# Performance work log

Hardware: AMD Instinct MI355X
Metric: run time of the kernel (lower is better)

Reference implementation:

```python
import jax, jax.numpy as jnp
import numpy as np

N = 50000   # num_entities
F = 300     # node feature dim
D = 128     # embedding_dim
H = 4       # heads
C = D // H  # per-head out channels (32)
E = 640000  # num edges
R = 200     # num_relations
L = 2       # num_layers
NEG_SLOPE = 0.2  # PyG GATv2Conv default


def setup_inputs() -> dict:
    key = jax.random.key(0)
    ks = jax.random.split(key, 14)
    s = 0.1
    return {
        "entity": jnp.arange(N, dtype=jnp.int32),
        "edge_index": jax.random.randint(ks[0], (2, E), 0, N, dtype=jnp.int32),
        "edge_type": jax.random.randint(ks[1], (E,), 0, R, dtype=jnp.int32),
        # learned parameters
        "node_features": jax.random.normal(ks[2], (N, F), jnp.float32) * s,   # entity_embedding table
        "rel_emb": jax.random.normal(ks[3], (R, D), jnp.float32) * s,          # relation_embedding
        "proj_w": jax.random.normal(ks[4], (F, D), jnp.float32) * s,           # project Linear
        "proj_b": jnp.zeros((D,), jnp.float32),
        # per-layer GATv2Conv params, stacked over L layers
        "w_l": jax.random.normal(ks[5], (L, D, H * C), jnp.float32) * s,       # lin_l weight
        "b_l": jnp.zeros((L, H * C), jnp.float32),
        "w_r": jax.random.normal(ks[6], (L, D, H * C), jnp.float32) * s,       # lin_r weight
        "b_r": jnp.zeros((L, H * C), jnp.float32),
        "w_e": jax.random.normal(ks[7], (L, D, H * C), jnp.float32) * s,       # lin_edge weight (no bias)
        "att": jax.random.normal(ks[8], (L, H, C), jnp.float32) * s,           # attention vector a
        "bias": jnp.zeros((L, H * C), jnp.float32),                             # output bias
    }


def _gatv2_layer(x, src, dst, edge_attr, w_l, b_l, w_r, b_r, w_e, att, bias):
    # x: [N, D], edge_attr: [E, D]
    x_l = (x @ w_l + b_l).reshape(N, H, C)
    x_r = (x @ w_r + b_r).reshape(N, H, C)
    e = (edge_attr @ w_e).reshape(E, H, C)
    # per-edge message (gather src/dst + edge), GATv2: leaky_relu BEFORE attention dot
    m = jax.nn.leaky_relu(x_l[src] + x_r[dst] + e, NEG_SLOPE)   # [E, H, C]
    logits = jnp.einsum('ehc,hc->eh', m, att)                    # [E, H]
    # segment softmax over edges grouped by destination node
    lmax = jax.ops.segment_max(logits, dst, num_segments=N)      # [N, H]
    ex = jnp.exp(logits - lmax[dst])                             # [E, H]
    denom = jax.ops.segment_sum(ex, dst, num_segments=N)         # [N, H]
    alpha = ex / denom[dst]                                      # [E, H]
    # scatter-aggregate messages x_l[src] weighted by alpha
    out = jax.ops.segment_sum(x_l[src] * alpha[:, :, None], dst, num_segments=N)  # [N, H, C]
    return out.reshape(N, H * C) + bias


def reference(entity, edge_index, edge_type, node_features, rel_emb,
              proj_w, proj_b, w_l, b_l, w_r, b_r, w_e, att, bias):
    x = node_features[entity]            # embedding lookup
    x = x @ proj_w + proj_b              # project to D
    edge_attr = rel_emb[edge_type]       # [E, D] (weights=False -> no edge_weight scaling)
    src, dst = edge_index[0], edge_index[1]
    for i in range(L):
        x = _gatv2_layer(x, src, dst, edge_attr,
                         w_l[i], b_l[i], w_r[i], b_r[i], w_e[i], att[i], bias[i])
        if i != L - 1:
            x = jax.nn.elu(x)            # dropout inactive (eval mode)
    return x
```

## Files before the change

kernel.cpp:

```cpp
#include <hip/hip_runtime.h>

#define NN 50000
#define FF 300
#define DD 128
#define HH 4
#define CC 32
#define EE 640000
#define RR 200
#define LL 2
#define SB ((NN + 255) / 256)
#define PK 320
#define WTOT (128 * PK + 4 * 128 * 128)
#define HB ((EE + 255) / 256)
#define WB ((WTOT + 255) / 256)
#define RB (LL * RR / 2)

typedef unsigned short u16;
typedef unsigned int u32;
typedef __attribute__((ext_vector_type(8))) short short8;
typedef __attribute__((ext_vector_type(4))) float floatx4;

__device__ __forceinline__ float bf2f(u16 u) {
    union { u32 i; float f; } v; v.i = ((u32)u) << 16; return v.f;
}
__device__ __forceinline__ u16 f2bf(float f) {
    u32 u = __float_as_uint(f);
    u32 r = (u >> 16) & 1u;
    u += 0x7fffu + r;
    return (u16)(u >> 16);
}
__device__ __forceinline__ void bf2x(u32 p, float& lo, float& hi) {
    lo = __uint_as_float(p << 16);
    hi = __uint_as_float(p & 0xffff0000u);
}

__device__ __forceinline__ int block_excl_scan(int v, int* lds4, int* total) {
    int lane = threadIdx.x & 63, wid = threadIdx.x >> 6;
    int x = v;
    #pragma unroll
    for (int off = 1; off < 64; off <<= 1) {
        int y = __shfl_up(x, off, 64);
        if (lane >= off) x += y;
    }
    if (lane == 63) lds4[wid] = x;
    __syncthreads();
    int add = 0;
    #pragma unroll
    for (int w = 0; w < 4; w++) add += (w < wid) ? lds4[w] : 0;
    *total = lds4[0] + lds4[1] + lds4[2] + lds4[3];
    return x + add - v;
}

__global__ __launch_bounds__(256)
void prep_kernel(const int* __restrict__ ei, int* __restrict__ counts,
                 const float* __restrict__ proj_w, const float* __restrict__ w_l,
                 const float* __restrict__ w_r, u16* __restrict__ wt,
                 const float* __restrict__ rel_emb, const float* __restrict__ w_e,
                 u16* __restrict__ erel)
{
    __shared__ float rv[2][DD];
    int b = blockIdx.x, tid = threadIdx.x;
    if (b < HB) {
        int e = b * 256 + tid;
        if (e < EE) atomicAdd(&counts[ei[EE + e]], 1);
    } else if (b < HB + WB) {
        int i = (b - HB) * 256 + tid;
        if (i < WTOT) {
            float v;
            if (i < 128 * PK) {
                int n = i / PK, k = i - n * PK;
                v = (k < FF) ? proj_w[(size_t)k * DD + n] : 0.f;
            } else {
                int j = i - 128 * PK;
                int seg = j >> 14;
                int r = j & 16383;
                int n = r >> 7, k = r & 127;
                const float* src = (seg < 2) ? (w_l + (size_t)seg * DD * DD)
                                             : (w_r + (size_t)(seg - 2) * DD * DD);
                v = src[(size_t)k * DD + n];
            }
            wt[i] = f2bf(v);
        }
    } else {
        int half = tid >> 7, d = tid & 127;
        int lr = (b - HB - WB) * 2 + half;
        int l = lr / RR, r = lr - l * RR;
        rv[half][d] = rel_emb[r * DD + d];
        __syncthreads();
        const float* W = w_e + (size_t)l * DD * DD;
        float acc = 0.f;
        #pragma unroll 8
        for (int k = 0; k < DD; k++) acc += rv[half][k] * W[k * DD + d];
        erel[(size_t)lr * DD + d] = f2bf(acc);
    }
}

template<bool ABF16, bool GATHER>
__global__ __launch_bounds__(256)
void gemm_mfma_kernel(const void* __restrict__ A_, const int* __restrict__ rowidx,
                      int lda, int K, int Ka, int ldb,
                      const u16* __restrict__ BT1, const float* __restrict__ bias1,
                      u16* __restrict__ C1,
                      const u16* __restrict__ BT2, const float* __restrict__ bias2,
                      u16* __restrict__ C2, int M)
{
    const u16*   BT   = (blockIdx.y == 0) ? BT1 : BT2;
    const float* bias = (blockIdx.y == 0) ? bias1 : bias2;
    u16*         Cout = (blockIdx.y == 0) ? C1 : C2;

    __shared__ u16 As[128][72];
    __shared__ u16 Bs[128][72];
    int tid  = threadIdx.x;
    int m0   = blockIdx.x * 128;
    int wave = tid >> 6, lane = tid & 63;
    int quad = lane >> 4, l16 = lane & 15;
    int wrow = (wave >> 1) * 64, wcol = (wave & 1) * 64;

    floatx4 acc[4][4];
    #pragma unroll
    for (int i = 0; i < 4; i++)
        #pragma unroll
        for (int j = 0; j < 4; j++) acc[i][j] = (floatx4){0.f, 0.f, 0.f, 0.f};

    int ar = tid >> 1, ah = tid & 1;
    int arow = m0 + ar;
    int rid = (arow < M) ? (GATHER ? rowidx[arow] : arow) : 0;

    for (int kk = 0; kk < K; kk += 64) {
        #pragma unroll
        for (int q = 0; q < 2; q++) {
            int kb = kk + ah * 32 + q * 16;
            u16 tmp[16];
            if (ABF16) {
                const u16* Ap = (const u16*)A_ + (size_t)rid * lda + kb;
                if (kb + 16 <= Ka) {
                    *(short8*)&tmp[0] = *(const short8*)Ap;
                    *(short8*)&tmp[8] = *(const short8*)(Ap + 8);
                } else {
                    #pragma unroll
                    for (int j = 0; j < 16; j++) tmp[j] = (kb + j < Ka) ? Ap[j] : (u16)0;
                }
            } else {
                const float* Ap = (const float*)A_ + (size_t)rid * lda + kb;
                if (kb + 16 <= Ka) {
                    #pragma unroll
                    for (int qq = 0; qq < 4; qq++) {
                        float4 f = *(const float4*)(Ap + qq * 4);
                        tmp[qq*4+0] = f2bf(f.x); tmp[qq*4+1] = f2bf(f.y);
                        tmp[qq*4+2] = f2bf(f.z); tmp[qq*4+3] = f2bf(f.w);
                    }
                } else {
                    #pragma unroll
                    for (int j = 0; j < 16; j++) tmp[j] = (kb + j < Ka) ? f2bf(Ap[j]) : (u16)0;
                }
            }
            *(short8*)&As[ar][ah * 32 + q * 16]     = *(short8*)&tmp[0];
            *(short8*)&As[ar][ah * 32 + q * 16 + 8] = *(short8*)&tmp[8];
        }
        {
            const u16* Bp = BT + (size_t)ar * ldb + kk + ah * 32;
            #pragma unroll
            for (int q = 0; q < 4; q++)
                *(short8*)&Bs[ar][ah * 32 + q * 8] = *(const short8*)(Bp + q * 8);
        }
        __syncthreads();
        #pragma unroll
        for (int ks = 0; ks < 2; ks++) {
            short8 af[4], bfr[4];
            #pragma unroll
            for (int i = 0; i < 4; i++)
                af[i] = *(const short8*)&As[wrow + i * 16 + l16][ks * 32 + quad * 8];
            #pragma unroll
            for (int j = 0; j < 4; j++)
                bfr[j] = *(const short8*)&Bs[wcol + j * 16 + l16][ks * 32 + quad * 8];
            #pragma unroll
            for (int i = 0; i < 4; i++)
                #pragma unroll
                for (int j = 0; j < 4; j++)
                    acc[i][j] = __builtin_amdgcn_mfma_f32_16x16x32_bf16(
                        af[i], bfr[j], acc[i][j], 0, 0, 0);
        }
        __syncthreads();
    }

    #pragma unroll
    for (int i = 0; i < 4; i++) {
        #pragma unroll
        for (int rr = 0; rr < 4; rr++) {
            int row = m0 + wrow + i * 16 + quad * 4 + rr;
            if (row < M) {
                #pragma unroll
                for (int j = 0; j < 4; j++) {
                    int col = wcol + j * 16 + l16;
                    Cout[(size_t)row * DD + col] = f2bf(acc[i][j][rr] + bias[col]);
                }
            }
        }
    }
}

__global__ __launch_bounds__(256)
void scan_local_kernel(const int* __restrict__ counts, int* __restrict__ offsets,
                       int* __restrict__ bsum)
{
    __shared__ int lds4[4];
    int i = blockIdx.x * 256 + threadIdx.x;
    int v = (i < NN) ? counts[i] : 0;
    int total;
    int ex = block_excl_scan(v, lds4, &total);
    if (i < NN) offsets[i] = ex;
    if (threadIdx.x == 0) bsum[blockIdx.x] = total;
}

__global__ __launch_bounds__(256)
void scan_bsum_kernel(int* __restrict__ bsum)
{
    __shared__ int lds4[4];
    int t = threadIdx.x;
    int v = (t < SB) ? bsum[t] : 0;
    int total;
    int ex = block_excl_scan(v, lds4, &total);
    if (t < SB) bsum[t] = ex;
}

__global__ __launch_bounds__(256)
void scan_add_kernel(int* __restrict__ offsets, const int* __restrict__ bsum)
{
    int i = blockIdx.x * 256 + threadIdx.x;
    if (i < NN) offsets[i] += bsum[i >> 8];
    if (i == 0) offsets[NN] = EE;
}

__global__ __launch_bounds__(256)
void scatter_kernel(const int* __restrict__ ei, const int* __restrict__ et,
                    const int* __restrict__ offsets,
                    int* __restrict__ fill, u32* __restrict__ dstorder)
{
    int e = blockIdx.x * 256 + threadIdx.x;
    if (e >= EE) return;
    int d = ei[EE + e];
    int pos = offsets[d] + atomicAdd(&fill[d], 1);
    dstorder[pos] = (u32)ei[e] | ((u32)et[e] << 16);
}

__global__ __launch_bounds__(256)
void node_kernel(const u32* __restrict__ dstorder, const int* __restrict__ offsets,
                 const u16* __restrict__ xl, const u16* __restrict__ xr,
                 const u16* __restrict__ erel, const float* __restrict__ att,
                 const float* __restrict__ bias,
                 u16* __restrict__ xnext, float* __restrict__ outp, int is_last)
{
    int tid  = threadIdx.x;
    int node = blockIdx.x * 4 + (tid >> 6);
    int lane = tid & 63;
    if (node >= NN) return;
    int g  = lane >> 4;
    int gl = lane & 15;
    int c0 = gl * 8;
    int beg = offsets[node], end = offsets[node + 1];

    float xrf[8], attf[8];
    {
        const u32* xp = (const u32*)&xr[(size_t)node * DD + c0];
        #pragma unroll
        for (int q = 0; q < 4; q++) bf2x(xp[q], xrf[q*2], xrf[q*2+1]);
        float4 a0 = *(const float4*)&att[c0];
        float4 a1 = *(const float4*)&att[c0 + 4];
        attf[0]=a0.x; attf[1]=a0.y; attf[2]=a0.z; attf[3]=a0.w;
        attf[4]=a1.x; attf[5]=a1.y; attf[6]=a1.z; attf[7]=a1.w;
    }

    float s = 0.f;
    float a[8];
    #pragma unroll
    for (int j = 0; j < 8; j++) a[j] = 0.f;

    for (int base = beg; base < end; base += 4) {
        int es = base + g;
        bool valid = es < end;
        u32 st = valid ? dstorder[es] : 0;
        int src = st & 0xffff;
        int typ = st >> 16;
        const u32* xp = (const u32*)&xl[(size_t)src * DD + c0];
        const u32* ep = (const u32*)&erel[(size_t)typ * DD + c0];
        u32 xv0 = xp[0], xv1 = xp[1], xv2 = xp[2], xv3 = xp[3];
        u32 ev0 = ep[0], ev1 = ep[1], ev2 = ep[2], ev3 = ep[3];
        float xf[8], ef[8];
        bf2x(xv0, xf[0], xf[1]); bf2x(xv1, xf[2], xf[3]);
        bf2x(xv2, xf[4], xf[5]); bf2x(xv3, xf[6], xf[7]);
        bf2x(ev0, ef[0], ef[1]); bf2x(ev1, ef[2], ef[3]);
        bf2x(ev2, ef[4], ef[5]); bf2x(ev3, ef[6], ef[7]);
        float p = 0.f;
        #pragma unroll
        for (int j = 0; j < 8; j++) {
            float m = xf[j] + xrf[j] + ef[j];
            m = fmaxf(m, 0.2f * m);
            p += m * attf[j];
        }
        p += __shfl_xor(p, 1, 64);
        p += __shfl_xor(p, 2, 64);
        float w = valid ? __expf(fminf(p, 60.f)) : 0.f;
        s += w;
        #pragma unroll
        for (int j = 0; j < 8; j++) a[j] += w * xf[j];
    }

    #pragma unroll
    for (int j = 0; j < 8; j++) {
        a[j] += __shfl_xor(a[j], 16, 64);
        a[j] += __shfl_xor(a[j], 32, 64);
    }
    s += __shfl_xor(s, 16, 64);
    s += __shfl_xor(s, 32, 64);

    if (lane < 16) {
        float rh = 1.f / fmaxf(s, 1e-30f);
        float4 b0 = *(const float4*)&bias[c0];
        float4 b1 = *(const float4*)&bias[c0 + 4];
        float bv[8] = {b0.x, b0.y, b0.z, b0.w, b1.x, b1.y, b1.z, b1.w};
        float v[8];
        #pragma unroll
        for (int j = 0; j < 8; j++) v[j] = a[j] * rh + bv[j];
        if (is_last) {
            float4* op = (float4*)&outp[(size_t)node * DD + c0];
            op[0] = make_float4(v[0], v[1], v[2], v[3]);
            op[1] = make_float4(v[4], v[5], v[6], v[7]);
        } else {
            u16 pk[8];
            #pragma unroll
            for (int j = 0; j < 8; j++) {
                float w2 = v[j] > 0.f ? v[j] : __expf(v[j]) - 1.f;
                pk[j] = f2bf(w2);
            }
            *(short8*)&xnext[(size_t)node * DD + c0] = *(short8*)pk;
        }
    }
}

extern "C" void kernel_launch(void* const* d_in, const int* in_sizes, int n_in,
                              void* d_out, int out_size, void* d_ws, size_t ws_size,
                              hipStream_t stream)
{
    const int*   entity        = (const int*)d_in[0];
    const int*   edge_index    = (const int*)d_in[1];
    const int*   edge_type     = (const int*)d_in[2];
    const float* node_features = (const float*)d_in[3];
    const float* rel_emb       = (const float*)d_in[4];
    const float* proj_w        = (const float*)d_in[5];
    const float* proj_b        = (const float*)d_in[6];
    const float* w_l           = (const float*)d_in[7];
    const float* b_l           = (const float*)d_in[8];
    const float* w_r           = (const float*)d_in[9];
    const float* b_r           = (const float*)d_in[10];
    const float* w_e           = (const float*)d_in[11];
    const float* att           = (const float*)d_in[12];
    const float* bias          = (const float*)d_in[13];

    u16*   xb      = (u16*)d_ws;
    u16*   xl      = xb + (size_t)NN * DD;
    u16*   xr      = xl + (size_t)NN * DD;
    u16*   erel    = xr + (size_t)NN * DD;
    u16*   wt      = erel + (size_t)LL * RR * DD;
    u32*   dstorder= (u32*)(wt + WTOT);
    int*   counts  = (int*)(dstorder + (size_t)EE);
    int*   fill    = counts + NN;
    int*   offsets = fill + NN;
    int*   bsum    = offsets + NN + 1;

    hipMemsetAsync(counts, 0, (size_t)NN * 2 * sizeof(int), stream);
    prep_kernel<<<HB + WB + RB, 256, 0, stream>>>(
        edge_index, counts, proj_w, w_l, w_r, wt, rel_emb, w_e, erel);

    scan_local_kernel<<<SB, 256, 0, stream>>>(counts, offsets, bsum);
    scan_bsum_kernel<<<1, 256, 0, stream>>>(bsum);
    scan_add_kernel<<<SB, 256, 0, stream>>>(offsets, bsum);
    scatter_kernel<<<(EE + 255) / 256, 256, 0, stream>>>(
        edge_index, edge_type, offsets, fill, dstorder);

    const u16* wtProj = wt;
    const int GB = (NN + 127) / 128;
    gemm_mfma_kernel<false, true><<<dim3(GB, 1), 256, 0, stream>>>(
        node_features, entity, FF, PK, FF, PK,
        wtProj, proj_b, xb, wtProj, proj_b, xb, NN);

    for (int l = 0; l < LL; l++) {
        const u16* wtl = wt + 128 * PK + l * 16384;
        const u16* wtr = wt + 128 * PK + 32768 + l * 16384;
        gemm_mfma_kernel<true, false><<<dim3(GB, 2), 256, 0, stream>>>(
            xb, nullptr, DD, DD, DD, DD,
            wtl, b_l + l * DD, xl,
            wtr, b_r + l * DD, xr, NN);

        node_kernel<<<(NN + 3) / 4, 256, 0, stream>>>(
            dstorder, offsets, xl, xr, erel + (size_t)l * RR * DD,
            att + (size_t)l * DD, bias + (size_t)l * DD,
            xb, (float*)d_out, l == LL - 1);
    }
}
```

Measured before the change: 338.7 us.

## Store xl and edge embeddings in fp32 and fold block-scan add into consumers

```diff
diff --git a/kernel.cpp b/kernel.cpp
--- a/kernel.cpp
+++ b/kernel.cpp
@@ -56,7 +56,7 @@
                  const float* __restrict__ proj_w, const float* __restrict__ w_l,
                  const float* __restrict__ w_r, u16* __restrict__ wt,
                  const float* __restrict__ rel_emb, const float* __restrict__ w_e,
-                 u16* __restrict__ erel)
+                 float* __restrict__ erel)
 {
     __shared__ float rv[2][DD];
     int b = blockIdx.x, tid = threadIdx.x;
@@ -91,22 +91,21 @@
         float acc = 0.f;
         #pragma unroll 8
         for (int k = 0; k < DD; k++) acc += rv[half][k] * W[k * DD + d];
-        erel[(size_t)lr * DD + d] = f2bf(acc);
-    }
-}
-
-template<bool ABF16, bool GATHER>
+        erel[(size_t)lr * DD + d] = acc;
+    }
+}
+
+template<bool ABF16, bool GATHER, bool OUT1F32>
 __global__ __launch_bounds__(256)
 void gemm_mfma_kernel(const void* __restrict__ A_, const int* __restrict__ rowidx,
                       int lda, int K, int Ka, int ldb,
                       const u16* __restrict__ BT1, const float* __restrict__ bias1,
-                      u16* __restrict__ C1,
+                      void* __restrict__ C1,
                       const u16* __restrict__ BT2, const float* __restrict__ bias2,
                       u16* __restrict__ C2, int M)
 {
     const u16*   BT   = (blockIdx.y == 0) ? BT1 : BT2;
     const float* bias = (blockIdx.y == 0) ? bias1 : bias2;
-    u16*         Cout = (blockIdx.y == 0) ? C1 : C2;
 
     __shared__ u16 As[128][72];
     __shared__ u16 Bs[128][72];
@@ -192,7 +191,13 @@
                 #pragma unroll
                 for (int j = 0; j < 4; j++) {
                     int col = wcol + j * 16 + l16;
-                    Cout[(size_t)row * DD + col] = f2bf(acc[i][j][rr] + bias[col]);
+                    float v = acc[i][j][rr] + bias[col];
+                    if (OUT1F32 && blockIdx.y == 0) {
+                        ((float*)C1)[(size_t)row * DD + col] = v;
+                    } else {
+                        u16* Cb = (blockIdx.y == 0) ? (u16*)C1 : C2;
+                        Cb[(size_t)row * DD + col] = f2bf(v);
+                    }
                 }
             }
         }
@@ -224,29 +229,22 @@
 }
 
 __global__ __launch_bounds__(256)
-void scan_add_kernel(int* __restrict__ offsets, const int* __restrict__ bsum)
-{
-    int i = blockIdx.x * 256 + threadIdx.x;
-    if (i < NN) offsets[i] += bsum[i >> 8];
-    if (i == 0) offsets[NN] = EE;
-}
-
-__global__ __launch_bounds__(256)
 void scatter_kernel(const int* __restrict__ ei, const int* __restrict__ et,
-                    const int* __restrict__ offsets,
+                    const int* __restrict__ offsets, const int* __restrict__ bsum,
                     int* __restrict__ fill, u32* __restrict__ dstorder)
 {
     int e = blockIdx.x * 256 + threadIdx.x;
     if (e >= EE) return;
     int d = ei[EE + e];
-    int pos = offsets[d] + atomicAdd(&fill[d], 1);
+    int pos = offsets[d] + bsum[d >> 8] + atomicAdd(&fill[d], 1);
     dstorder[pos] = (u32)ei[e] | ((u32)et[e] << 16);
 }
 
 __global__ __launch_bounds__(256)
 void node_kernel(const u32* __restrict__ dstorder, const int* __restrict__ offsets,
-                 const u16* __restrict__ xl, const u16* __restrict__ xr,
-                 const u16* __restrict__ erel, const float* __restrict__ att,
+                 const int* __restrict__ bsum,
+                 const float* __restrict__ xl, const u16* __restrict__ xr,
+                 const float* __restrict__ erel, const float* __restrict__ att,
                  const float* __restrict__ bias,
                  u16* __restrict__ xnext, float* __restrict__ outp, int is_last)
 {
@@ -257,7 +255,8 @@
     int g  = lane >> 4;
     int gl = lane & 15;
     int c0 = gl * 8;
-    int beg = offsets[node], end = offsets[node + 1];
+    int beg = offsets[node] + bsum[node >> 8];
+    int end = (node == NN - 1) ? EE : offsets[node + 1] + bsum[(node + 1) >> 8];
 
     float xrf[8], attf[8];
     {
@@ -281,15 +280,14 @@
         u32 st = valid ? dstorder[es] : 0;
         int src = st & 0xffff;
         int typ = st >> 16;
-        const u32* xp = (const u32*)&xl[(size_t)src * DD + c0];
-        const u32* ep = (const u32*)&erel[(size_t)typ * DD + c0];
-        u32 xv0 = xp[0], xv1 = xp[1], xv2 = xp[2], xv3 = xp[3];
-        u32 ev0 = ep[0], ev1 = ep[1], ev2 = ep[2], ev3 = ep[3];
-        float xf[8], ef[8];
-        bf2x(xv0, xf[0], xf[1]); bf2x(xv1, xf[2], xf[3]);
-        bf2x(xv2, xf[4], xf[5]); bf2x(xv3, xf[6], xf[7]);
-        bf2x(ev0, ef[0], ef[1]); bf2x(ev1, ef[2], ef[3]);
-        bf2x(ev2, ef[4], ef[5]); bf2x(ev3, ef[6], ef[7]);
+        const float* xp = xl + (size_t)src * DD + c0;
+        const float* ep = erel + (size_t)typ * DD + c0;
+        float4 x0 = *(const float4*)xp;
+        float4 x1 = *(const float4*)(xp + 4);
+        float4 e0 = *(const float4*)ep;
+        float4 e1 = *(const float4*)(ep + 4);
+        float xf[8] = {x0.x, x0.y, x0.z, x0.w, x1.x, x1.y, x1.z, x1.w};
+        float ef[8] = {e0.x, e0.y, e0.z, e0.w, e1.x, e1.y, e1.z, e1.w};
         float p = 0.f;
         #pragma unroll
         for (int j = 0; j < 8; j++) {
@@ -357,15 +355,15 @@
     const float* bias          = (const float*)d_in[13];
 
     u16*   xb      = (u16*)d_ws;
-    u16*   xl      = xb + (size_t)NN * DD;
-    u16*   xr      = xl + (size_t)NN * DD;
-    u16*   erel    = xr + (size_t)NN * DD;
-    u16*   wt      = erel + (size_t)LL * RR * DD;
+    float* xlf     = (float*)(xb + (size_t)NN * DD);
+    u16*   xr      = (u16*)(xlf + (size_t)NN * DD);
+    float* erel    = (float*)(xr + (size_t)NN * DD);
+    u16*   wt      = (u16*)(erel + (size_t)LL * RR * DD);
     u32*   dstorder= (u32*)(wt + WTOT);
     int*   counts  = (int*)(dstorder + (size_t)EE);
     int*   fill    = counts + NN;
     int*   offsets = fill + NN;
-    int*   bsum    = offsets + NN + 1;
+    int*   bsum    = offsets + NN;
 
     hipMemsetAsync(counts, 0, (size_t)NN * 2 * sizeof(int), stream);
     prep_kernel<<<HB + WB + RB, 256, 0, stream>>>(
@@ -373,26 +371,25 @@
 
     scan_local_kernel<<<SB, 256, 0, stream>>>(counts, offsets, bsum);
     scan_bsum_kernel<<<1, 256, 0, stream>>>(bsum);
-    scan_add_kernel<<<SB, 256, 0, stream>>>(offsets, bsum);
     scatter_kernel<<<(EE + 255) / 256, 256, 0, stream>>>(
-        edge_index, edge_type, offsets, fill, dstorder);
+        edge_index, edge_type, offsets, bsum, fill, dstorder);
 
     const u16* wtProj = wt;
     const int GB = (NN + 127) / 128;
-    gemm_mfma_kernel<false, true><<<dim3(GB, 1), 256, 0, stream>>>(
+    gemm_mfma_kernel<false, true, false><<<dim3(GB, 1), 256, 0, stream>>>(
         node_features, entity, FF, PK, FF, PK,
         wtProj, proj_b, xb, wtProj, proj_b, xb, NN);
 
     for (int l = 0; l < LL; l++) {
         const u16* wtl = wt + 128 * PK + l * 16384;
         const u16* wtr = wt + 128 * PK + 32768 + l * 16384;
-        gemm_mfma_kernel<true, false><<<dim3(GB, 2), 256, 0, stream>>>(
+        gemm_mfma_kernel<true, false, true><<<dim3(GB, 2), 256, 0, stream>>>(
             xb, nullptr, DD, DD, DD, DD,
-            wtl, b_l + l * DD, xl,
+            wtl, b_l + l * DD, xlf,
             wtr, b_r + l * DD, xr, NN);
 
         node_kernel<<<(NN + 3) / 4, 256, 0, stream>>>(
-            dstorder, offsets, xl, xr, erel + (size_t)l * RR * DD,
+            dstorder, offsets, bsum, xlf, xr, erel + (size_t)l * RR * DD,
             att + (size_t)l * DD, bias + (size_t)l * DD,
             xb, (float*)d_out, l == LL - 1);
     }
```

New measurement: 381.6 us. 1.13x slower.
